# Kernel tuning notes

Hardware: AMD Instinct MI355X
Metric: run time of the kernel (lower is better)

## Reference

```python
import jax, jax.numpy as jnp
import numpy as np

B, T, F, H, O = 4096, 64, 512, 64, 2

def setup_inputs() -> dict:
    key = jax.random.key(0)
    ks = jax.random.split(key, 7)
    s_ih = 1.0 / np.sqrt(H)
    return {
        "x": jax.random.normal(ks[0], (B, T, F), dtype=jnp.float32),
        # PyTorch LSTM params: weight_ih_l0 [4H, F], weight_hh_l0 [4H, H], biases [4H]
        "W_ih": jax.random.uniform(ks[1], (4 * H, F), jnp.float32, -s_ih, s_ih),
        "W_hh": jax.random.uniform(ks[2], (4 * H, H), jnp.float32, -s_ih, s_ih),
        "b_ih": jax.random.uniform(ks[3], (4 * H,), jnp.float32, -s_ih, s_ih),
        "b_hh": jax.random.uniform(ks[4], (4 * H,), jnp.float32, -s_ih, s_ih),
        "W_fc": jax.random.uniform(ks[5], (O, H), jnp.float32, -s_ih, s_ih),
        "b_fc": jax.random.uniform(ks[6], (O,), jnp.float32, -s_ih, s_ih),
    }

def _lstm_last_h(x, W_ih, W_hh, b_ih, b_hh):
    # Precompute input contributions for all timesteps: [B, T, 4H]
    xg = jnp.einsum('btf,gf->btg', x, W_ih) + (b_ih + b_hh)
    h0 = jnp.zeros((x.shape[0], W_hh.shape[1]), x.dtype)
    c0 = jnp.zeros_like(h0)

    def step(carry, xt):
        h, c = carry
        gates = xt + h @ W_hh.T  # [B, 4H]
        i, f, g, o = jnp.split(gates, 4, axis=-1)  # PyTorch gate order i,f,g,o
        i = jax.nn.sigmoid(i)
        f = jax.nn.sigmoid(f)
        g = jnp.tanh(g)
        o = jax.nn.sigmoid(o)
        c_new = f * c + i * g
        h_new = o * jnp.tanh(c_new)
        return (h_new, c_new), None

    (hT, _), _ = jax.lax.scan(step, (h0, c0), jnp.swapaxes(xg, 0, 1))  # scan over T
    return hT  # [B, H] = out[:, -1, :]

def reference(x, W_ih, W_hh, b_ih, b_hh, W_fc, b_fc):
    hT = _lstm_last_h(x, W_ih, W_hh, b_ih, b_hh)
    return hT @ W_fc.T + b_fc  # [B, O]
```

## Files before the change

kernel.cpp:

```cpp
#include <hip/hip_runtime.h>

#define B_SZ 4096
#define T_SZ 64
#define F_SZ 512
#define H_SZ 64
#define BR 8
#define WIH_ELEMS (256 * 512)

typedef _Float16 f16x4 __attribute__((ext_vector_type(4)));
typedef _Float16 f16x8 __attribute__((ext_vector_type(8)));
typedef float f32x4 __attribute__((ext_vector_type(4)));

__device__ __forceinline__ float fast_rcp(float x) { return __builtin_amdgcn_rcpf(x); }
__device__ __forceinline__ float sigm(float x) { return fast_rcp(1.0f + __expf(-x)); }
__device__ __forceinline__ float tanh_f(float x) {
  x = fminf(15.0f, fmaxf(-15.0f, x));
  float e = __expf(2.0f * x);
  return (e - 1.0f) * fast_rcp(e + 1.0f);
}

__global__ void transcode_f16(const float* __restrict__ Wih, const float* __restrict__ Whh,
                              _Float16* __restrict__ ws) {
  const int i4 = (blockIdx.x * 256 + threadIdx.x) * 4;
  if (i4 < WIH_ELEMS) {
    float4 v = *(const float4*)(Wih + i4);
    ws[i4] = (_Float16)v.x; ws[i4+1] = (_Float16)v.y; ws[i4+2] = (_Float16)v.z; ws[i4+3] = (_Float16)v.w;
  } else {
    const int j4 = i4 - WIH_ELEMS;
    float4 v = *(const float4*)(Whh + j4);
    _Float16* w2 = ws + WIH_ELEMS;
    w2[j4] = (_Float16)v.x; w2[j4+1] = (_Float16)v.y; w2[j4+2] = (_Float16)v.z; w2[j4+3] = (_Float16)v.w;
  }
}

__global__ __launch_bounds__(256, 2)
void lstm_fused(const float* __restrict__ x, const _Float16* __restrict__ ws,
                const float* __restrict__ bih, const float* __restrict__ bhh,
                const float* __restrict__ Wfc, const float* __restrict__ bfc,
                float* __restrict__ out)
{
  __shared__ __align__(16) _Float16 Ast[2][64 * 64];
  __shared__ __align__(16) _Float16 xgb[8][8][256];
  __shared__ __align__(16) _Float16 hbuf[2][8][72];
  __shared__ float cb[8][64];
  __shared__ float h32[8][64];

  const int tid  = threadIdx.x;
  const int wv   = tid >> 6;
  const int lane = tid & 63;
  const int ln   = lane & 15;
  const int kg   = lane >> 4;
  const int br0  = blockIdx.x * BR;
  const int u    = wv * 16 + ln;

  const _Float16* Wihh = ws;
  const _Float16* Whhh = ws + WIH_ELEMS;

  for (int i = tid; i < 2 * 8 * 72; i += 256) (&hbuf[0][0][0])[i] = (_Float16)0.0f;
  for (int i = tid; i < 8 * 64; i += 256) (&cb[0][0])[i] = 0.0f;

  f16x8 whhf[4][2];
  #pragma unroll
  for (int g = 0; g < 4; ++g)
    #pragma unroll
    for (int k2 = 0; k2 < 2; ++k2)
      whhf[g][k2] = *(const f16x8*)(Whhh + (size_t)((g * 4 + wv) * 16 + ln) * H_SZ
                                         + kg * 8 + k2 * 32);
  float bsum[4];
  #pragma unroll
  for (int g = 0; g < 4; ++g) bsum[g] = bih[g * 64 + u] + bhh[g * 64 + u];

  auto loadX = [&](float4 (&p)[4], int t2) {
    const int tt = t2 < 64 ? t2 : 63;
    const int c2 = tt >> 3, kq = tt & 7;
    #pragma unroll
    for (int j = 0; j < 4; ++j) {
      const int row = wv * 16 + 4 * j + (lane >> 4);
      const float* sp = x + (size_t)(br0 + (row & 7)) * (T_SZ * F_SZ)
                          + (size_t)(c2 * 8 + (row >> 3)) * F_SZ + kq * 64 + (lane & 15) * 4;
      p[j] = *(const float4*)sp;
    }
  };
  auto stageW = [&](const float4 (&p)[4], int buf) {
    #pragma unroll
    for (int j = 0; j < 4; ++j) {
      const int row = wv * 16 + 4 * j + (lane >> 4);
      const int c16 = lane & 15;
      const int pg  = (c16 >> 1) ^ (row & 7);
      f16x4 h = {(_Float16)p[j].x, (_Float16)p[j].y, (_Float16)p[j].z, (_Float16)p[j].w};
      *(f16x4*)&Ast[buf][row * 64 + pg * 8 + (c16 & 1) * 4] = h;
    }
  };
  auto loadB = [&](f16x8 (&b)[4][2], int kq) {
    #pragma unroll
    for (int g = 0; g < 4; ++g)
      #pragma unroll
      for (int ks = 0; ks < 2; ++ks)
        b[g][ks] = *(const f16x8*)(Wihh + (size_t)((g * 4 + wv) * 16 + ln) * F_SZ
                                        + kq * 64 + ks * 32 + kg * 8);
  };

  f32x4 acc[4][4];
  auto consume = [&](const f16x8 (&b)[4][2], int buf) {
    #pragma unroll
    for (int ks = 0; ks < 2; ++ks)
      #pragma unroll
      for (int mt = 0; mt < 4; ++mt) {
        const int m    = mt * 16 + ln;
        const int phys = (ks * 4 + kg) ^ (ln & 7);
        f16x8 af = *(const f16x8*)&Ast[buf][m * 64 + phys * 8];
        #pragma unroll
        for (int g = 0; g < 4; ++g)
          acc[mt][g] = __builtin_amdgcn_mfma_f32_16x16x32_f16(af, b[g][ks], acc[mt][g], 0, 0, 0);
      }
  };

  auto scanStep = [&](int st) {
    const int sl = st & 7, half = sl & 1;
    f16x8 ah0 = (f16x8){0, 0, 0, 0, 0, 0, 0, 0};
    f16x8 ah1 = (f16x8){0, 0, 0, 0, 0, 0, 0, 0};
    if ((ln >> 3) == half) {
      const _Float16* hr = &hbuf[st & 1][ln & 7][0];
      ah0 = *(const f16x8*)(hr + kg * 8);
      ah1 = *(const f16x8*)(hr + kg * 8 + 32);
    }
    const bool val = (kg >> 1) == half;
    f32x4 gf[4];
    if (val) {
      #pragma unroll
      for (int r = 0; r < 4; ++r) {
        f16x4 xv = *(const f16x4*)&xgb[sl][(kg & 1) * 4 + r][u * 4];
        gf[0][r] = (float)xv[0]; gf[1][r] = (float)xv[1];
        gf[2][r] = (float)xv[2]; gf[3][r] = (float)xv[3];
      }
    } else {
      #pragma unroll
      for (int g = 0; g < 4; ++g) gf[g] = (f32x4){0.0f, 0.0f, 0.0f, 0.0f};
    }
    #pragma unroll
    for (int g = 0; g < 4; ++g) {
      gf[g] = __builtin_amdgcn_mfma_f32_16x16x32_f16(ah0, whhf[g][0], gf[g], 0, 0, 0);
      gf[g] = __builtin_amdgcn_mfma_f32_16x16x32_f16(ah1, whhf[g][1], gf[g], 0, 0, 0);
    }
    if (val) {
      const int b0 = (kg & 1) * 4;
      #pragma unroll
      for (int r = 0; r < 4; ++r) {
        const float iv = sigm(gf[0][r] + bsum[0]);
        const float fv = sigm(gf[1][r] + bsum[1]);
        const float gv = tanh_f(gf[2][r] + bsum[2]);
        const float ov = sigm(gf[3][r] + bsum[3]);
        const float cn = fv * cb[b0 + r][u] + iv * gv;
        cb[b0 + r][u] = cn;
        const float hn = ov * tanh_f(cn);
        hbuf[(st + 1) & 1][b0 + r][u] = (_Float16)hn;
        if (st == T_SZ - 1) h32[b0 + r][u] = hn;
      }
    }
  };

  auto handoff = [&]() {
    #pragma unroll
    for (int mt = 0; mt < 4; ++mt) {
      const int sl2  = mt * 2 + (kg >> 1);
      const int brow = (kg & 1) * 4;
      #pragma unroll
      for (int r = 0; r < 4; ++r) {
        f16x4 h4 = {(_Float16)acc[mt][0][r], (_Float16)acc[mt][1][r],
                    (_Float16)acc[mt][2][r], (_Float16)acc[mt][3][r]};
        *(f16x4*)&xgb[sl2][brow + r][u * 4] = h4;
      }
    }
    asm volatile("s_waitcnt lgkmcnt(0)" ::: "memory");
    __builtin_amdgcn_s_barrier();
    #pragma unroll
    for (int mt = 0; mt < 4; ++mt)
      #pragma unroll
      for (int g = 0; g < 4; ++g) acc[mt][g] = (f32x4){0.0f, 0.0f, 0.0f, 0.0f};
  };

  f16x8 bfr[4][2];
  float4 xpA[4], xpB[4];

#define ITER(tau, SRC, DST)                                                  \
  do {                                                                       \
    const int kk_ = (tau) & 7;                                               \
    loadB(bfr, kk_);                                                         \
    loadX(DST, (tau) + 2);                                                   \
    __builtin_amdgcn_sched_barrier(0);                                       \
    consume(bfr, (tau) & 1);          \
    if ((tau) >= 8) scanStep((tau) - 8);                                     \
    __builtin_amdgcn_sched_barrier(0);                                       \
    stageW(SRC, ((tau) + 1) & 1);              \
    asm volatile("s_waitcnt lgkmcnt(0)" ::: "memory");                       \
    __builtin_amdgcn_s_barrier();                                            \
    if (kk_ == 7) handoff();                                                 \
  } while (0)

  loadX(xpA, 0);
  stageW(xpA, 0);
  loadX(xpA, 1);
  __syncthreads();

  #pragma unroll
  for (int mt = 0; mt < 4; ++mt)
    #pragma unroll
    for (int g = 0; g < 4; ++g) acc[mt][g] = (f32x4){0.0f, 0.0f, 0.0f, 0.0f};

  for (int p = 0; p < 32; ++p) {
    ITER(2 * p,     xpA, xpB);
    ITER(2 * p + 1, xpB, xpA);
  }
#undef ITER

  for (int s2 = 56; s2 < 64; ++s2) {
    scanStep(s2);
    asm volatile("s_waitcnt lgkmcnt(0)" ::: "memory");
    __builtin_amdgcn_s_barrier();
  }

  __syncthreads();
  if (tid < 16) {
    const int r = tid >> 1, j = tid & 1;
    float a = bfc[j];
    #pragma unroll
    for (int uu = 0; uu < 64; ++uu) a += h32[r][uu] * Wfc[j * 64 + uu];
    out[(size_t)(br0 + r) * 2 + j] = a;
  }
}

extern "C" void kernel_launch(void* const* d_in, const int* in_sizes, int n_in,
                              void* d_out, int out_size, void* d_ws, size_t ws_size,
                              hipStream_t stream) {
  const float* x   = (const float*)d_in[0];
  const float* Wih = (const float*)d_in[1];
  const float* Whh = (const float*)d_in[2];
  const float* bih = (const float*)d_in[3];
  const float* bhh = (const float*)d_in[4];
  const float* Wfc = (const float*)d_in[5];
  const float* bfc = (const float*)d_in[6];
  float* out = (float*)d_out;
  _Float16* ws = (_Float16*)d_ws;

  transcode_f16<<<dim3(144), dim3(256), 0, stream>>>(Wih, Whh, ws);
  lstm_fused<<<dim3(B_SZ / BR), dim3(256), 0, stream>>>(x, ws, bih, bhh, Wfc, bfc, out);
}
```

Measured before the change: 176.7 us.

## Retile input GEMM stage to 32x128 chunks so W_ih fragments reuse across two steps

Changes the per-iteration A tile from 64 rows by 64 K-columns to 32 rows by 128 K-columns. The W_ih B-fragments (now 4 k-slices) are loaded only on even iterations and reused for the two row-halves of the 64-row block on consecutive iterations. This halves the global/L2 loads of f16 W_ih per block. In exchange it doubles the B-fragment register footprint, which risks lower occupancy or spills under launch_bounds(256,2).

```diff
diff --git a/kernel.cpp b/kernel.cpp
--- a/kernel.cpp
+++ b/kernel.cpp
@@ -39,7 +39,7 @@
                 const float* __restrict__ Wfc, const float* __restrict__ bfc,
                 float* __restrict__ out)
 {
-  __shared__ __align__(16) _Float16 Ast[2][64 * 64];
+  __shared__ __align__(16) _Float16 Ast[2][32 * 128];
   __shared__ __align__(16) _Float16 xgb[8][8][256];
   __shared__ __align__(16) _Float16 hbuf[2][8][72];
   __shared__ float cb[8][64];
@@ -72,46 +72,62 @@
 
   auto loadX = [&](float4 (&p)[4], int t2) {
     const int tt = t2 < 64 ? t2 : 63;
-    const int c2 = tt >> 3, kq = tt & 7;
+    const int c2 = tt >> 3, kq = (tt & 7) >> 1, mh = tt & 1;
     #pragma unroll
     for (int j = 0; j < 4; ++j) {
-      const int row = wv * 16 + 4 * j + (lane >> 4);
-      const float* sp = x + (size_t)(br0 + (row & 7)) * (T_SZ * F_SZ)
-                          + (size_t)(c2 * 8 + (row >> 3)) * F_SZ + kq * 64 + (lane & 15) * 4;
+      const int lr = wv * 8 + 2 * j + (lane >> 5);
+      const float* sp = x + (size_t)(br0 + (lr & 7)) * (T_SZ * F_SZ)
+                          + (size_t)(c2 * 8 + mh * 4 + (lr >> 3)) * F_SZ
+                          + kq * 128 + (lane & 31) * 4;
       p[j] = *(const float4*)sp;
     }
   };
   auto stageW = [&](const float4 (&p)[4], int buf) {
     #pragma unroll
     for (int j = 0; j < 4; ++j) {
-      const int row = wv * 16 + 4 * j + (lane >> 4);
-      const int c16 = lane & 15;
-      const int pg  = (c16 >> 1) ^ (row & 7);
+      const int lr = wv * 8 + 2 * j + (lane >> 5);
+      const int p31 = lane & 31;
+      const int pg  = (p31 >> 1) ^ (lr & 7);
       f16x4 h = {(_Float16)p[j].x, (_Float16)p[j].y, (_Float16)p[j].z, (_Float16)p[j].w};
-      *(f16x4*)&Ast[buf][row * 64 + pg * 8 + (c16 & 1) * 4] = h;
-    }
-  };
-  auto loadB = [&](f16x8 (&b)[4][2], int kq) {
+      *(f16x4*)&Ast[buf][lr * 128 + pg * 8 + (p31 & 1) * 4] = h;
+    }
+  };
+  auto loadB = [&](f16x8 (&b)[4][4], int kq) {
     #pragma unroll
     for (int g = 0; g < 4; ++g)
       #pragma unroll
-      for (int ks = 0; ks < 2; ++ks)
+      for (int ks = 0; ks < 4; ++ks)
         b[g][ks] = *(const f16x8*)(Wihh + (size_t)((g * 4 + wv) * 16 + ln) * F_SZ
-                                        + kq * 64 + ks * 32 + kg * 8);
+                                        + kq * 128 + ks * 32 + kg * 8);
   };
 
   f32x4 acc[4][4];
-  auto consume = [&](const f16x8 (&b)[4][2], int buf) {
-    #pragma unroll
-    for (int ks = 0; ks < 2; ++ks)
-      #pragma unroll
-      for (int mt = 0; mt < 4; ++mt) {
-        const int m    = mt * 16 + ln;
+  f16x8 bfr[4][4];
+
+  auto consume0 = [&](int buf) {
+    #pragma unroll
+    for (int ks = 0; ks < 4; ++ks)
+      #pragma unroll
+      for (int tt = 0; tt < 2; ++tt) {
+        const int lr = tt * 16 + ln;
         const int phys = (ks * 4 + kg) ^ (ln & 7);
-        f16x8 af = *(const f16x8*)&Ast[buf][m * 64 + phys * 8];
+        f16x8 af = *(const f16x8*)&Ast[buf][lr * 128 + phys * 8];
         #pragma unroll
         for (int g = 0; g < 4; ++g)
-          acc[mt][g] = __builtin_amdgcn_mfma_f32_16x16x32_f16(af, b[g][ks], acc[mt][g], 0, 0, 0);
+          acc[tt][g] = __builtin_amdgcn_mfma_f32_16x16x32_f16(af, bfr[g][ks], acc[tt][g], 0, 0, 0);
+      }
+  };
+  auto consume1 = [&](int buf) {
+    #pragma unroll
+    for (int ks = 0; ks < 4; ++ks)
+      #pragma unroll
+      for (int tt = 0; tt < 2; ++tt) {
+        const int lr = tt * 16 + ln;
+        const int phys = (ks * 4 + kg) ^ (ln & 7);
+        f16x8 af = *(const f16x8*)&Ast[buf][lr * 128 + phys * 8];
+        #pragma unroll
+        for (int g = 0; g < 4; ++g)
+          acc[2 + tt][g] = __builtin_amdgcn_mfma_f32_16x16x32_f16(af, bfr[g][ks], acc[2 + tt][g], 0, 0, 0);
       }
   };
 
@@ -179,22 +195,20 @@
       for (int g = 0; g < 4; ++g) acc[mt][g] = (f32x4){0.0f, 0.0f, 0.0f, 0.0f};
   };
 
-  f16x8 bfr[4][2];
   float4 xpA[4], xpB[4];
 
-#define ITER(tau, SRC, DST)                                                  \
-  do {                                                                       \
-    const int kk_ = (tau) & 7;                                               \
-    loadB(bfr, kk_);                                                         \
-    loadX(DST, (tau) + 2);                                                   \
-    __builtin_amdgcn_sched_barrier(0);                                       \
-    consume(bfr, (tau) & 1);          \
-    if ((tau) >= 8) scanStep((tau) - 8);                                     \
-    __builtin_amdgcn_sched_barrier(0);                                       \
-    stageW(SRC, ((tau) + 1) & 1);              \
-    asm volatile("s_waitcnt lgkmcnt(0)" ::: "memory");                       \
-    __builtin_amdgcn_s_barrier();                                            \
-    if (kk_ == 7) handoff();                                                 \
+#define ITER(tau, SRC, DST)                                                    \
+  do {                                                                         \
+    if (((tau) & 1) == 0) loadB(bfr, ((tau) & 7) >> 1);                        \
+    loadX(DST, (tau) + 2);                                                     \
+    __builtin_amdgcn_sched_barrier(0);                                         \
+    if (((tau) & 1) == 0) consume0((tau) & 1); else consume1((tau) & 1);       \
+    if ((tau) >= 8) scanStep((tau) - 8);                                       \
+    __builtin_amdgcn_sched_barrier(0);                                         \
+    stageW(SRC, ((tau) + 1) & 1);                                              \
+    asm volatile("s_waitcnt lgkmcnt(0)" ::: "memory");                         \
+    __builtin_amdgcn_s_barrier();                                              \
+    if (((tau) & 7) == 7) handoff();                                           \
   } while (0)
 
   loadX(xpA, 0);
```

Measured after the change: 244.1 us. 1.38x slower.
